# Kernel optimization log

Hardware: AMD Instinct MI355X
Metric: run time of the kernel (lower is better)

## Reference

```python
import jax, jax.numpy as jnp
import numpy as np

B, L, HID = 16, 512, 768
HEADS, M = 12, 4
EMB, BLK, NER, NCLS = 768, 8, 6, 97


def setup_inputs() -> dict:
    key = jax.random.key(0)
    ks = jax.random.split(key, 10)
    return {
        "sequence_output": jax.random.normal(ks[0], (B, L, HID), jnp.float32),
        "attention": jax.random.uniform(ks[1], (B, HEADS, L, L), jnp.float32),
        "entity_pos": jax.random.randint(ks[2], (B, 2, M), 0, L - 2),
        "hs_ner_tags": jax.random.uniform(ks[3], (B, NER), jnp.float32),
        "ts_ner_tags": jax.random.uniform(ks[4], (B, NER), jnp.float32),
        "Wh": jax.random.normal(ks[5], (EMB, 2 * HID + NER), jnp.float32) * 0.02,
        "bh": jnp.zeros((EMB,), jnp.float32),
        "Wt": jax.random.normal(ks[6], (EMB, 2 * HID + NER), jnp.float32) * 0.02,
        "bt": jnp.zeros((EMB,), jnp.float32),
        "Wb": jax.random.normal(ks[7], (NCLS, EMB * BLK), jnp.float32) * 0.02,
        "bb": jnp.zeros((NCLS,), jnp.float32),
    }


def reference(sequence_output, attention, entity_pos, hs_ner_tags, ts_ner_tags,
              Wh, bh, Wt, bt, Wb, bb):
    b_idx = jnp.arange(B)[:, None, None]            # [B,1,1]
    starts = entity_pos + 1                         # [B,2,M] (all < L by construction)

    # entity embeddings: gather mention token embeddings, logsumexp-pool over mentions
    ment_emb = sequence_output[b_idx, starts]       # [B,2,M,HID]
    ent_emb = jax.scipy.special.logsumexp(ment_emb, axis=2)  # [B,2,HID]

    # entity attentions: gather mention attention rows, mean-pool over mentions
    attn_t = attention.transpose(0, 2, 1, 3)        # [B,L,HEADS,L]
    ment_att = attn_t[b_idx, starts]                # [B,2,M,HEADS,L]
    ent_att = ment_att.mean(axis=2)                 # [B,2,HEADS,L]

    hs, ts = ent_emb[:, 0], ent_emb[:, 1]           # [B,HID]
    h_att, t_att = ent_att[:, 0], ent_att[:, 1]     # [B,HEADS,L]

    ht_att = (h_att * t_att).mean(axis=1)           # [B,L]
    ht_att = ht_att / (ht_att.sum(axis=1, keepdims=True) + 1e-5)
    rs = jnp.einsum('bld,bl->bd', sequence_output, ht_att)  # [B,HID]

    hs2 = jnp.tanh(jnp.concatenate([hs, rs, hs_ner_tags], axis=1) @ Wh.T + bh)
    ts2 = jnp.tanh(jnp.concatenate([ts, rs, ts_ner_tags], axis=1) @ Wt.T + bt)

    b1 = hs2.reshape(B, EMB // BLK, BLK)
    b2 = ts2.reshape(B, EMB // BLK, BLK)
    bl = (b1[:, :, :, None] * b2[:, :, None, :]).reshape(B, EMB * BLK)
    logits = bl @ Wb.T + bb                         # [B, NCLS]
    return logits
```

## Files before the change

### kernel.cpp

```cpp
#include <hip/hip_runtime.h>
#include <math.h>

#define B 16
#define L 512
#define HID 768
#define HEADS 12
#define M 4
#define EMB 768
#define BLK 8
#define NER 6
#define NCLS 97
#define CAT (2*HID + NER)
#define EB (EMB*BLK)

__global__ void k_entemb(const float* __restrict__ seq, const int* __restrict__ epos,
                         float* __restrict__ ent) {
    int b = blockIdx.x, e = blockIdx.y;
    int s0 = epos[(b*2+e)*M + 0] + 1;
    int s1 = epos[(b*2+e)*M + 1] + 1;
    int s2 = epos[(b*2+e)*M + 2] + 1;
    int s3 = epos[(b*2+e)*M + 3] + 1;
    const float* base = seq + (size_t)b*L*HID;
    for (int d = threadIdx.x; d < HID; d += blockDim.x) {
        float v0 = base[(size_t)s0*HID + d];
        float v1 = base[(size_t)s1*HID + d];
        float v2 = base[(size_t)s2*HID + d];
        float v3 = base[(size_t)s3*HID + d];
        float mx = fmaxf(fmaxf(v0, v1), fmaxf(v2, v3));
        float s = expf(v0-mx) + expf(v1-mx) + expf(v2-mx) + expf(v3-mx);
        ent[((size_t)e*B + b)*HID + d] = mx + logf(s);
    }
}

__global__ void k_htatt(const float* __restrict__ att, const int* __restrict__ epos,
                        float* __restrict__ ht) {
    int b = blockIdx.x;
    int l = threadIdx.x;
    int s0[M], s1[M];
    for (int m = 0; m < M; ++m) {
        s0[m] = epos[(b*2+0)*M + m] + 1;
        s1[m] = epos[(b*2+1)*M + m] + 1;
    }
    float raw = 0.f;
    for (int h = 0; h < HEADS; ++h) {
        const float* ah = att + ((size_t)b*HEADS + h)*L*L;
        float a0 = 0.f, a1 = 0.f;
        for (int m = 0; m < M; ++m) {
            a0 += ah[(size_t)s0[m]*L + l];
            a1 += ah[(size_t)s1[m]*L + l];
        }
        raw += (a0*0.25f) * (a1*0.25f);
    }
    raw *= (1.0f/HEADS);
    float v = raw;
    for (int off = 32; off; off >>= 1) v += __shfl_down(v, off);
    __shared__ float warp_s[8];
    __shared__ float tot;
    int wid = threadIdx.x >> 6, lane = threadIdx.x & 63;
    if (lane == 0) warp_s[wid] = v;
    __syncthreads();
    if (threadIdx.x == 0) {
        float t = 0.f;
        for (int i = 0; i < 8; ++i) t += warp_s[i];
        tot = t + 1e-5f;
    }
    __syncthreads();
    ht[b*L + l] = raw / tot;
}

__global__ void k_rs(const float* __restrict__ seq, const float* __restrict__ ht,
                     float* __restrict__ rs) {
    int b = blockIdx.x;
    int d = blockIdx.y*128 + threadIdx.x;
    __shared__ float hl[L];
    for (int l = threadIdx.x; l < L; l += 128) hl[l] = ht[b*L + l];
    __syncthreads();
    const float* sp = seq + (size_t)b*L*HID + d;
    float acc = 0.f;
    for (int l = 0; l < L; ++l) acc += sp[(size_t)l*HID] * hl[l];
    rs[b*HID + d] = acc;
}

__global__ void k_proj(const float* __restrict__ Wh, const float* __restrict__ bh,
                       const float* __restrict__ Wt, const float* __restrict__ bt,
                       const float* __restrict__ ent, const float* __restrict__ rs,
                       const float* __restrict__ hner, const float* __restrict__ tner,
                       float* __restrict__ out) {
    int t = blockIdx.y;
    int wid = threadIdx.x >> 6, lane = threadIdx.x & 63;
    int j = blockIdx.x*4 + wid;
    const float* W    = t ? Wt : Wh;
    const float* bias = t ? bt : bh;
    const float* e0   = ent + (size_t)t*B*HID;
    const float* ner  = t ? tner : hner;
    const float* wrow = W + (size_t)j*CAT;

    float acc[B];
    for (int b = 0; b < B; ++b) acc[b] = 0.f;

    for (int i = 0; i < 25; ++i) {
        int k = i*64 + lane;
        if (k < CAT) {
            float w = wrow[k];
            if (k < HID) {
                for (int b = 0; b < B; ++b) acc[b] += w * e0[b*HID + k];
            } else if (k < 2*HID) {
                int kk = k - HID;
                for (int b = 0; b < B; ++b) acc[b] += w * rs[b*HID + kk];
            } else {
                int kk = k - 2*HID;
                for (int b = 0; b < B; ++b) acc[b] += w * ner[b*NER + kk];
            }
        }
    }
    for (int off = 32; off; off >>= 1)
        for (int b = 0; b < B; ++b) acc[b] += __shfl_down(acc[b], off);
    if (lane == 0) {
        float bj = bias[j];
        for (int b = 0; b < B; ++b)
            out[((size_t)t*B + b)*EMB + j] = tanhf(acc[b] + bj);
    }
}

__global__ void k_bl(const float* __restrict__ hs2, const float* __restrict__ ts2,
                     float* __restrict__ bl) {
    int b = blockIdx.x;
    for (int idx = threadIdx.x; idx < EB; idx += blockDim.x) {
        int g = idx >> 6;
        int r = (idx >> 3) & 7;
        int c = idx & 7;
        bl[(size_t)b*EB + idx] = hs2[b*EMB + g*BLK + r] * ts2[b*EMB + g*BLK + c];
    }
}

__global__ void k_logits(const float* __restrict__ Wb, const float* __restrict__ bb,
                         const float* __restrict__ bl, float* __restrict__ out) {
    int c = blockIdx.x;
    const float* wr = Wb + (size_t)c*EB;
    float acc[B];
    for (int b = 0; b < B; ++b) acc[b] = 0.f;
    for (int k = threadIdx.x; k < EB; k += blockDim.x) {
        float w = wr[k];
        for (int b = 0; b < B; ++b) acc[b] += w * bl[(size_t)b*EB + k];
    }
    int wid = threadIdx.x >> 6, lane = threadIdx.x & 63;
    for (int off = 32; off; off >>= 1)
        for (int b = 0; b < B; ++b) acc[b] += __shfl_down(acc[b], off);
    __shared__ float part[4][B];
    if (lane == 0)
        for (int b = 0; b < B; ++b) part[wid][b] = acc[b];
    __syncthreads();
    if (threadIdx.x < B) {
        int b = threadIdx.x;
        float s = part[0][b] + part[1][b] + part[2][b] + part[3][b];
        out[b*NCLS + c] = s + bb[c];
    }
}

extern "C" void kernel_launch(void* const* d_in, const int* in_sizes, int n_in,
                              void* d_out, int out_size, void* d_ws, size_t ws_size,
                              hipStream_t stream) {
    const float* seq  = (const float*)d_in[0];
    const float* att  = (const float*)d_in[1];
    const int*   epos = (const int*)  d_in[2];
    const float* hner = (const float*)d_in[3];
    const float* tner = (const float*)d_in[4];
    const float* Wh   = (const float*)d_in[5];
    const float* bh   = (const float*)d_in[6];
    const float* Wt   = (const float*)d_in[7];
    const float* bt   = (const float*)d_in[8];
    const float* Wb   = (const float*)d_in[9];
    const float* bb   = (const float*)d_in[10];
    float* out = (float*)d_out;

    float* ws   = (float*)d_ws;
    float* ent  = ws;
    float* rs   = ent  + 2*B*HID;
    float* ht   = rs   + B*HID;
    float* proj = ht   + B*L;
    float* bl   = proj + 2*B*EMB;

    k_entemb<<<dim3(B, 2), 256, 0, stream>>>(seq, epos, ent);
    k_htatt <<<dim3(B),   512, 0, stream>>>(att, epos, ht);
    k_rs    <<<dim3(B, HID/128), 128, 0, stream>>>(seq, ht, rs);
    k_proj  <<<dim3(EMB/4, 2), 256, 0, stream>>>(Wh, bh, Wt, bt, ent, rs, hner, tner, proj);
    k_bl    <<<dim3(B),   256, 0, stream>>>(proj, proj + (size_t)B*EMB, bl);
    k_logits<<<dim3(NCLS),256, 0, stream>>>(Wb, bb, bl, out);
}
```

Measured before the change: 350.6 us.

## Fuse front kernels, split rs reduction, stage activations in LDS, fold bilinear into logits

Merges entity-embedding pooling and attention pooling into one kernel and splits the weighted sequence reduction over L into 8 chunks with float4 loads for more parallelism. The projection kernel now reduces the chunk partials while staging activations in shared memory, and splits the batch across a grid dimension. The bilinear product is computed inside the logits kernel instead of being materialised, and blocks are widened to 512 threads. The cost is redundant recomputation of the hs*ts products per class and a large shared-memory buffer in the projection kernel.

```diff
diff --git a/kernel.cpp b/kernel.cpp
--- a/kernel.cpp
+++ b/kernel.cpp
@@ -12,147 +12,167 @@
 #define NCLS 97
 #define CAT (2*HID + NER)
 #define EB (EMB*BLK)
-
-__global__ void k_entemb(const float* __restrict__ seq, const int* __restrict__ epos,
-                         float* __restrict__ ent) {
-    int b = blockIdx.x, e = blockIdx.y;
-    int s0 = epos[(b*2+e)*M + 0] + 1;
-    int s1 = epos[(b*2+e)*M + 1] + 1;
-    int s2 = epos[(b*2+e)*M + 2] + 1;
-    int s3 = epos[(b*2+e)*M + 3] + 1;
-    const float* base = seq + (size_t)b*L*HID;
-    for (int d = threadIdx.x; d < HID; d += blockDim.x) {
-        float v0 = base[(size_t)s0*HID + d];
-        float v1 = base[(size_t)s1*HID + d];
-        float v2 = base[(size_t)s2*HID + d];
-        float v3 = base[(size_t)s3*HID + d];
-        float mx = fmaxf(fmaxf(v0, v1), fmaxf(v2, v3));
-        float s = expf(v0-mx) + expf(v1-mx) + expf(v2-mx) + expf(v3-mx);
-        ent[((size_t)e*B + b)*HID + d] = mx + logf(s);
-    }
-}
-
-__global__ void k_htatt(const float* __restrict__ att, const int* __restrict__ epos,
-                        float* __restrict__ ht) {
+#define NCH 8
+#define CATP 1544
+
+__global__ void k_front(const float* __restrict__ seq, const float* __restrict__ att,
+                        const int* __restrict__ epos,
+                        float* __restrict__ ent, float* __restrict__ ht) {
     int b = blockIdx.x;
+    __shared__ int ss[2][M];
+    if (threadIdx.x < 2*M) {
+        int e = threadIdx.x >> 2, m = threadIdx.x & 3;
+        ss[e][m] = epos[(b*2+e)*M + m] + 1;
+    }
+    __syncthreads();
+
     int l = threadIdx.x;
-    int s0[M], s1[M];
-    for (int m = 0; m < M; ++m) {
-        s0[m] = epos[(b*2+0)*M + m] + 1;
-        s1[m] = epos[(b*2+1)*M + m] + 1;
-    }
     float raw = 0.f;
     for (int h = 0; h < HEADS; ++h) {
         const float* ah = att + ((size_t)b*HEADS + h)*L*L;
         float a0 = 0.f, a1 = 0.f;
+        #pragma unroll
         for (int m = 0; m < M; ++m) {
-            a0 += ah[(size_t)s0[m]*L + l];
-            a1 += ah[(size_t)s1[m]*L + l];
+            a0 += ah[(size_t)ss[0][m]*L + l];
+            a1 += ah[(size_t)ss[1][m]*L + l];
         }
-        raw += (a0*0.25f) * (a1*0.25f);
-    }
-    raw *= (1.0f/HEADS);
+        raw += a0*a1;
+    }
+    raw *= (1.f/(M*M*HEADS));
     float v = raw;
     for (int off = 32; off; off >>= 1) v += __shfl_down(v, off);
-    __shared__ float warp_s[8];
+    __shared__ float wsum[8];
     __shared__ float tot;
     int wid = threadIdx.x >> 6, lane = threadIdx.x & 63;
-    if (lane == 0) warp_s[wid] = v;
+    if (lane == 0) wsum[wid] = v;
     __syncthreads();
     if (threadIdx.x == 0) {
         float t = 0.f;
-        for (int i = 0; i < 8; ++i) t += warp_s[i];
+        #pragma unroll
+        for (int i = 0; i < 8; ++i) t += wsum[i];
         tot = t + 1e-5f;
     }
     __syncthreads();
     ht[b*L + l] = raw / tot;
-}
-
-__global__ void k_rs(const float* __restrict__ seq, const float* __restrict__ ht,
-                     float* __restrict__ rs) {
-    int b = blockIdx.x;
-    int d = blockIdx.y*128 + threadIdx.x;
-    __shared__ float hl[L];
-    for (int l = threadIdx.x; l < L; l += 128) hl[l] = ht[b*L + l];
-    __syncthreads();
-    const float* sp = seq + (size_t)b*L*HID + d;
-    float acc = 0.f;
-    for (int l = 0; l < L; ++l) acc += sp[(size_t)l*HID] * hl[l];
-    rs[b*HID + d] = acc;
-}
-
+
+    const float* base = seq + (size_t)b*L*HID;
+    for (int idx = threadIdx.x; idx < 2*HID; idx += 512) {
+        int e = (idx >= HID) ? 1 : 0;
+        int d = idx - e*HID;
+        float v0 = base[(size_t)ss[e][0]*HID + d];
+        float v1 = base[(size_t)ss[e][1]*HID + d];
+        float v2 = base[(size_t)ss[e][2]*HID + d];
+        float v3 = base[(size_t)ss[e][3]*HID + d];
+        float mx = fmaxf(fmaxf(v0, v1), fmaxf(v2, v3));
+        float s = expf(v0-mx) + expf(v1-mx) + expf(v2-mx) + expf(v3-mx);
+        ent[((size_t)e*B + b)*HID + d] = mx + logf(s);
+    }
+}
+
+__global__ void k_rs_part(const float* __restrict__ seq, const float* __restrict__ ht,
+                          float* __restrict__ part) {
+    int b = blockIdx.x, ch = blockIdx.y;
+    const int LC = L/NCH;
+    __shared__ float hl[L/NCH];
+    if (threadIdx.x < LC) hl[threadIdx.x] = ht[b*L + ch*LC + threadIdx.x];
+    __syncthreads();
+    const float4* sp = (const float4*)(seq + (size_t)b*L*HID + (size_t)ch*LC*HID);
+    float4 acc = make_float4(0.f, 0.f, 0.f, 0.f);
+    for (int i = 0; i < LC; ++i) {
+        float4 vv = sp[i*(HID/4) + threadIdx.x];
+        float w = hl[i];
+        acc.x += vv.x*w; acc.y += vv.y*w; acc.z += vv.z*w; acc.w += vv.w*w;
+    }
+    ((float4*)(part + ((size_t)ch*B + b)*HID))[threadIdx.x] = acc;
+}
+
+__launch_bounds__(512)
 __global__ void k_proj(const float* __restrict__ Wh, const float* __restrict__ bh,
                        const float* __restrict__ Wt, const float* __restrict__ bt,
-                       const float* __restrict__ ent, const float* __restrict__ rs,
+                       const float* __restrict__ ent, const float* __restrict__ part,
                        const float* __restrict__ hner, const float* __restrict__ tner,
                        float* __restrict__ out) {
-    int t = blockIdx.y;
+    int t = blockIdx.y, zh = blockIdx.z;
+    __shared__ float act[8*CATP];
+    const float* e0  = ent + (size_t)t*B*HID;
+    const float* ner = t ? tner : hner;
+    for (int bi = 0; bi < 8; ++bi) {
+        int gb = zh*8 + bi;
+        for (int k = threadIdx.x; k < CAT; k += 512) {
+            float v;
+            if (k < HID) {
+                v = e0[gb*HID + k];
+            } else if (k < 2*HID) {
+                int kk = k - HID;
+                float s = 0.f;
+                #pragma unroll
+                for (int c = 0; c < NCH; ++c) s += part[((size_t)c*B + gb)*HID + kk];
+                v = s;
+            } else {
+                v = ner[gb*NER + (k - 2*HID)];
+            }
+            act[bi*CATP + k] = v;
+        }
+    }
+    __syncthreads();
+
     int wid = threadIdx.x >> 6, lane = threadIdx.x & 63;
-    int j = blockIdx.x*4 + wid;
-    const float* W    = t ? Wt : Wh;
-    const float* bias = t ? bt : bh;
-    const float* e0   = ent + (size_t)t*B*HID;
-    const float* ner  = t ? tner : hner;
-    const float* wrow = W + (size_t)j*CAT;
-
-    float acc[B];
-    for (int b = 0; b < B; ++b) acc[b] = 0.f;
-
+    int j = blockIdx.x*8 + wid;
+    const float* wrow = (t ? Wt : Wh) + (size_t)j*CAT;
+    float acc[8];
+    #pragma unroll
+    for (int b = 0; b < 8; ++b) acc[b] = 0.f;
     for (int i = 0; i < 25; ++i) {
         int k = i*64 + lane;
         if (k < CAT) {
             float w = wrow[k];
-            if (k < HID) {
-                for (int b = 0; b < B; ++b) acc[b] += w * e0[b*HID + k];
-            } else if (k < 2*HID) {
-                int kk = k - HID;
-                for (int b = 0; b < B; ++b) acc[b] += w * rs[b*HID + kk];
-            } else {
-                int kk = k - 2*HID;
-                for (int b = 0; b < B; ++b) acc[b] += w * ner[b*NER + kk];
-            }
+            #pragma unroll
+            for (int b = 0; b < 8; ++b) acc[b] += w * act[b*CATP + k];
         }
     }
     for (int off = 32; off; off >>= 1)
-        for (int b = 0; b < B; ++b) acc[b] += __shfl_down(acc[b], off);
+        #pragma unroll
+        for (int b = 0; b < 8; ++b) acc[b] += __shfl_down(acc[b], off);
     if (lane == 0) {
-        float bj = bias[j];
-        for (int b = 0; b < B; ++b)
-            out[((size_t)t*B + b)*EMB + j] = tanhf(acc[b] + bj);
-    }
-}
-
-__global__ void k_bl(const float* __restrict__ hs2, const float* __restrict__ ts2,
-                     float* __restrict__ bl) {
-    int b = blockIdx.x;
-    for (int idx = threadIdx.x; idx < EB; idx += blockDim.x) {
-        int g = idx >> 6;
-        int r = (idx >> 3) & 7;
-        int c = idx & 7;
-        bl[(size_t)b*EB + idx] = hs2[b*EMB + g*BLK + r] * ts2[b*EMB + g*BLK + c];
-    }
-}
-
+        float bj = (t ? bt : bh)[j];
+        #pragma unroll
+        for (int b = 0; b < 8; ++b)
+            out[((size_t)t*B + zh*8 + b)*EMB + j] = tanhf(acc[b] + bj);
+    }
+}
+
+__launch_bounds__(512)
 __global__ void k_logits(const float* __restrict__ Wb, const float* __restrict__ bb,
-                         const float* __restrict__ bl, float* __restrict__ out) {
+                         const float* __restrict__ proj, float* __restrict__ out) {
     int c = blockIdx.x;
     const float* wr = Wb + (size_t)c*EB;
+    const float* ph = proj;
+    const float* pt = proj + (size_t)B*EMB;
     float acc[B];
+    #pragma unroll
     for (int b = 0; b < B; ++b) acc[b] = 0.f;
-    for (int k = threadIdx.x; k < EB; k += blockDim.x) {
+    for (int k = threadIdx.x; k < EB; k += 512) {
+        int g = k >> 6, r = (k >> 3) & 7, cc = k & 7;
         float w = wr[k];
-        for (int b = 0; b < B; ++b) acc[b] += w * bl[(size_t)b*EB + k];
+        int o = g*8;
+        #pragma unroll
+        for (int b = 0; b < B; ++b)
+            acc[b] += w * ph[b*EMB + o + r] * pt[b*EMB + o + cc];
     }
     int wid = threadIdx.x >> 6, lane = threadIdx.x & 63;
     for (int off = 32; off; off >>= 1)
+        #pragma unroll
         for (int b = 0; b < B; ++b) acc[b] += __shfl_down(acc[b], off);
-    __shared__ float part[4][B];
+    __shared__ float partl[8][B];
     if (lane == 0)
-        for (int b = 0; b < B; ++b) part[wid][b] = acc[b];
+        #pragma unroll
+        for (int b = 0; b < B; ++b) partl[wid][b] = acc[b];
     __syncthreads();
     if (threadIdx.x < B) {
         int b = threadIdx.x;
-        float s = part[0][b] + part[1][b] + part[2][b] + part[3][b];
+        float s = 0.f;
+        #pragma unroll
+        for (int w = 0; w < 8; ++w) s += partl[w][b];
         out[b*NCLS + c] = s + bb[c];
     }
 }
@@ -175,15 +195,12 @@
 
     float* ws   = (float*)d_ws;
     float* ent  = ws;
-    float* rs   = ent  + 2*B*HID;
-    float* ht   = rs   + B*HID;
-    float* proj = ht   + B*L;
-    float* bl   = proj + 2*B*EMB;
-
-    k_entemb<<<dim3(B, 2), 256, 0, stream>>>(seq, epos, ent);
-    k_htatt <<<dim3(B),   512, 0, stream>>>(att, epos, ht);
-    k_rs    <<<dim3(B, HID/128), 128, 0, stream>>>(seq, ht, rs);
-    k_proj  <<<dim3(EMB/4, 2), 256, 0, stream>>>(Wh, bh, Wt, bt, ent, rs, hner, tner, proj);
-    k_bl    <<<dim3(B),   256, 0, stream>>>(proj, proj + (size_t)B*EMB, bl);
-    k_logits<<<dim3(NCLS),256, 0, stream>>>(Wb, bb, bl, out);
-}
+    float* ht   = ent  + 2*B*HID;
+    float* part = ht   + B*L;
+    float* proj = part + (size_t)NCH*B*HID;
+
+    k_front  <<<dim3(B),          512, 0, stream>>>(seq, att, epos, ent, ht);
+    k_rs_part<<<dim3(B, NCH),     192, 0, stream>>>(seq, ht, part);
+    k_proj   <<<dim3(EMB/8, 2, 2),512, 0, stream>>>(Wh, bh, Wt, bt, ent, part, hner, tner, proj);
+    k_logits <<<dim3(NCLS),       512, 0, stream>>>(Wb, bb, proj, out);
+}
```

Result: faster. 338.3 us (-3.5%).
